# Kernel tuning notes

Measured on AMD Instinct MI355X. Metric: run time of the kernel, lower is better.

Reference implementation:

```python
import jax, jax.numpy as jnp
import numpy as np
from jax import lax

# Kernel / geometry constants matching init_kwargs
KZ, KX, KY = 9, 15, 15          # PSF support
STRIDE = (1, 1, 1)              # scale = (zscale, xscale, yscale)
Z_PAD = (KZ - 1 + 1) // 2       # 4
X_PAD = (KX - 1 + 1) // 2       # 7
Y_PAD = (KY - 1 + 1) // 2       # 7


def _dist(n):
    # |idx - n//2|, matching _distance_from_center
    return jnp.abs(jnp.arange(n, dtype=jnp.float32) - n // 2)


def gen_psf(bet_xy, bet_z, alpha):
    b = bet_xy.shape[0]
    zd = _dist(KZ)                                  # [KZ]
    xd = _dist(KX)
    yd = _dist(KY)
    # gen_distance_plane: dp[i, j] = xd[j]^2 + yd[i]^2  (shape [KY, KX])
    dp = yd[:, None] ** 2 + xd[None, :] ** 2
    # gen_2dnorm: [b, KY, KX]
    bxy = bet_xy[:, None, None]
    lat = jnp.exp(-dp[None] / (2.0 * bxy ** 2)) / (2.0 * jnp.pi * bxy ** 2)
    # gen_1dnorm: [b, KZ]
    bz = bet_z[:, None]
    ax = jnp.exp(-(zd[None] ** 2) / (2.0 * bz ** 2)) / (jnp.sqrt(2.0 * jnp.pi) * bz)
    # psf = exp(log(lateral) + log(axial)) == lateral * axial  -> [b, 1, KZ, KY, KX]
    psf = lat[:, None, None, :, :] * ax[:, None, :, None, None]
    # double_exp mode
    psf = 1.0 - jnp.exp(-alpha[:, None, None, None, None] * psf)
    return psf / jnp.sum(psf)


def reference(x, bet_xy, bet_z, alpha):
    # x: [B, 1, Z, X, Y]; original computes dense conv3d giving [B, B, ...] and
    # keeps only the diagonal _x[b, b]. That is mathematically a per-sample
    # (grouped) convolution, implemented here without the O(B) redundancy.
    psf = gen_psf(bet_xy, bet_z, alpha)             # [B, 1, KZ, KY, KX]
    B = x.shape[0]
    xin = jnp.transpose(x, (1, 0, 2, 3, 4))         # [1, B, Z, X, Y]
    out = lax.conv_general_dilated(
        xin, psf,
        window_strides=STRIDE,
        padding=[(Z_PAD, Z_PAD), (X_PAD, X_PAD), (Y_PAD, Y_PAD)],
        dimension_numbers=("NCDHW", "OIDHW", "NCDHW"),
        feature_group_count=B,
    )                                               # [1, B, Z', X', Y']
    return jnp.transpose(out, (1, 0, 2, 3, 4))      # [B, 1, Z', X', Y']


def setup_inputs() -> dict:
    key = jax.random.key(0)
    k1, k2, k3, k4 = jax.random.split(key, 4)
    B = 4
    x = jax.random.normal(k1, (B, 1, 32, 192, 192), dtype=jnp.float32)
    bet_xy = 1.0 + 2.0 * jax.random.uniform(k2, (B,), dtype=jnp.float32)   # in [1, 3)
    bet_z = 1.0 + 2.0 * jax.random.uniform(k3, (B,), dtype=jnp.float32)    # in [1, 3)
    alpha = 1.0 + 9.0 * jax.random.uniform(k4, (B,), dtype=jnp.float32)    # in [1, 10)
    return {"x": x, "bet_xy": bet_xy, "bet_z": bet_z, "alpha": alpha}
```

## Files before the change

### kernel.cpp

```cpp
#include <hip/hip_runtime.h>
#include <math.h>

#define B_ 4
#define D_ 32
#define H_ 192
#define W_ 192
#define HW_ (H_ * W_)

#define NT 5

#define TW 48
#define TH 12
#define NTHR 256
#define ZCHUNK 16
#define NP (ZCHUNK + 8)

#define XT_H 26
#define XT_COLS 62
#define XT_W 64
#define XT_CELLS (XT_H * XT_COLS)
#define NSEC 7
#define XT_SZ (XT_H * XT_W)

#define R2_PL (TH * XT_W)
#define RBUF (NT * R2_PL)

#define SMEM_WORDS (2 * XT_SZ + 2 * RBUF + 16)

#define NTAPS (B_ * 9 * 15 * 15)

__device__ inline float4 f4fma(float c, float4 a, float4 d) {
    d.x = fmaf(c, a.x, d.x); d.y = fmaf(c, a.y, d.y);
    d.z = fmaf(c, a.z, d.z); d.w = fmaf(c, a.w, d.w);
    return d;
}
__device__ inline float4 f4add(float4 a, float4 b) {
    a.x += b.x; a.y += b.y; a.z += b.z; a.w += b.w; return a;
}
__device__ inline float rfl(float x) {
    return __int_as_float(__builtin_amdgcn_readfirstlane(__float_as_int(x)));
}

__global__ __launch_bounds__(NTHR)
void conv_kernel(const float* __restrict__ x,
                 const float* __restrict__ bet_xy,
                 const float* __restrict__ bet_z,
                 const float* __restrict__ alpha,
                 float* __restrict__ out) {
    __shared__ __align__(16) float smem[SMEM_WORDS];
    float* xtb = smem;
    float* Rb  = smem + 2 * XT_SZ;
    float* red = smem;
    float* ct  = smem + 512;

    const int t  = threadIdx.x;
    const int w0 = blockIdx.x * TW;
    const int h0 = blockIdx.y * TH;
    const int bz = blockIdx.z;
    const int b  = bz & 3;
    const int z0 = (bz >> 2) * ZCHUNK;
    const float INV = 0.3989422804014327f;

    float local = 0.f;
#pragma unroll
    for (int s = 0; s < 32; ++s) {
        int idx = t + s * NTHR;
        if (idx < NTAPS) {
            int bb = idx / 2025;
            int r  = idx % 2025;
            int dz = r / 225;
            int r2 = r % 225;
            int dh = r2 / 15;
            int dw = r2 % 15;
            float bxy = bet_xy[bb], bzv = bet_z[bb], al = alpha[bb];
            float zd = (float)(dz - 4), hd = (float)(dh - 7), wd = (float)(dw - 7);
            float az = expf(-zd * zd / (2.f * bzv * bzv)) * (INV / bzv);
            float gh = expf(-hd * hd / (2.f * bxy * bxy)) * (INV / bxy);
            float gw = expf(-wd * wd / (2.f * bxy * bxy)) * (INV / bxy);
            local += 1.f - expf(-al * az * gh * gw);
        }
    }
    red[t] = local;
    __syncthreads();
    for (int s = 128; s > 0; s >>= 1) {
        if (t < s) red[t] += red[t + s];
        __syncthreads();
    }
    const float S = red[0];
    __syncthreads();

    if (t < NT * 13) {
        int n = t / 13;
        int k = t % 13;
        float bxy = bet_xy[b], bzv = bet_z[b], al = alpha[b];
        if (k < 8) {
            float d = (float)k;
            float g = expf(-d * d / (2.f * bxy * bxy)) * (INV / bxy);
            float p = g;
            for (int q = 0; q < n; ++q) p *= g;
            ct[n * 16 + k] = p;
        } else {
            float d = (float)(k - 8);
            float az = expf(-d * d / (2.f * bzv * bzv)) * (INV / bzv);
            float base = al * az;
            float p = base;
            for (int q = 0; q < n; ++q) p *= base;
            const float facs[NT] = {1.f, 2.f, 6.f, 24.f, 120.f};
            float sign = (n & 1) ? -1.f : 1.f;
            ct[n * 16 + k] = sign * p / (facs[n] * S);
        }
    }
    __syncthreads();

    float cg_[NT][8], cz_[NT][5];
#pragma unroll
    for (int n = 0; n < NT; ++n) {
#pragma unroll
        for (int k = 0; k < 8; ++k) cg_[n][k] = rfl(ct[n * 16 + k]);
#pragma unroll
        for (int k = 0; k < 5; ++k) cz_[n][k] = rfl(ct[n * 16 + 8 + k]);
    }
    __syncthreads();

    const float* xb = x + (size_t)b * (D_ * HW_);
    int goff[NSEC], loff[NSEC];
#pragma unroll
    for (int k = 0; k < NSEC; ++k) {
        int i = t + k * NTHR;
        int r = i / XT_COLS, c = i - r * XT_COLS;
        int gh = h0 + r - 7, gw = w0 + c - 7;
        bool ok = (i < XT_CELLS) && gh >= 0 && gh < H_ && gw >= 0 && gw < W_;
        goff[k] = ok ? (gh * W_ + gw) : -1;
        loff[k] = (i < XT_CELLS) ? (r * XT_W + c) : (XT_SZ - 1);
    }
    if (t < XT_H * 2) {
        int r = t >> 1, c = 62 + (t & 1);
        xtb[r * XT_W + c] = 0.f;
        xtb[XT_SZ + r * XT_W + c] = 0.f;
    }
    {
        int zi0 = z0 - 4;
        if (zi0 >= 0) {
#pragma unroll
            for (int k = 0; k < NSEC; ++k) {
                float v = 0.f;
                if (goff[k] >= 0) v = xb[(size_t)zi0 * HW_ + goff[k]];
                xtb[loff[k]] = v;
            }
        }
    }

    const int bid = blockIdx.x + (int)gridDim.x * (blockIdx.y + (int)gridDim.y * blockIdx.z);
    const int rt  = (t + ((bid & 1) << 7)) & (NTHR - 1);

    const bool s1act = (rt < 192);
    const bool s2on = (rt >= 64);
    const int l2 = rt - 64;
    const int s2ro = l2 >> 4, s2cg = l2 & 15;
    const bool s2store = s2on && (s2cg < 12);

    float4 acc[9];
#pragma unroll
    for (int k = 0; k < 9; ++k) acc[k] = make_float4(0.f, 0.f, 0.f, 0.f);

#pragma unroll 1
    for (int p = 0; p <= NP; ++p) {
        __syncthreads();

        const int zi = z0 - 4 + p;
        const bool do_s1 = (p < NP) && (zi >= 0) && (zi < D_) && s1act;
        const int  zn    = zi + 1;
        const bool pvalid = (p + 1 < NP) && (zn >= 0) && (zn < D_);

        float pv[NSEC];
        if (pvalid) {
            const float* xp = xb + (size_t)zn * HW_;
#pragma unroll
            for (int k = 0; k < NSEC; ++k) pv[k] = (goff[k] >= 0) ? xp[goff[k]] : 0.f;
        }

        if (do_s1) {
            const float4* x4 = (const float4*)(xtb + (p & 1) * XT_SZ + 4 * rt);
            float4* R4 = (float4*)(Rb + (p & 1) * RBUF) + rt;
            float4 ctr = x4[7 * 16];
            float4 sp[7];
#pragma unroll
            for (int k = 1; k <= 7; ++k)
                sp[k - 1] = f4add(x4[(7 - k) * 16], x4[(7 + k) * 16]);
#pragma unroll
            for (int n = 0; n < NT; ++n) {
                float c0 = cg_[n][0];
                float4 a;
                a.x = c0 * ctr.x; a.y = c0 * ctr.y;
                a.z = c0 * ctr.z; a.w = c0 * ctr.w;
#pragma unroll
                for (int k = 1; k <= 7; ++k) a = f4fma(cg_[n][k], sp[k - 1], a);
                R4[n * (R2_PL / 4)] = a;
            }
        }

        if (p >= 1 && s2on) {
            const int ziq = zi - 1;
            if (ziq >= 0 && ziq < D_) {
                const float4* R4 = (const float4*)(Rb + ((p - 1) & 1) * RBUF) + l2;
#pragma unroll
                for (int n = 0; n < NT; ++n) {
                    float win[20];
#pragma unroll
                    for (int i = 0; i < 5; ++i) {
                        float4 a = R4[n * (R2_PL / 4) + i];
                        win[4 * i]     = a.x; win[4 * i + 1] = a.y;
                        win[4 * i + 2] = a.z; win[4 * i + 3] = a.w;
                    }
                    float c0 = cg_[n][0];
                    float4 qv;
                    qv.x = c0 * win[7];  qv.y = c0 * win[8];
                    qv.z = c0 * win[9];  qv.w = c0 * win[10];
#pragma unroll
                    for (int k = 1; k <= 7; ++k) {
                        float c = cg_[n][k];
                        qv.x = fmaf(c, win[7 - k]  + win[7 + k],  qv.x);
                        qv.y = fmaf(c, win[8 - k]  + win[8 + k],  qv.y);
                        qv.z = fmaf(c, win[9 - k]  + win[9 + k],  qv.z);
                        qv.w = fmaf(c, win[10 - k] + win[10 + k], qv.w);
                    }
                    acc[4] = f4fma(cz_[n][0], qv, acc[4]);
#pragma unroll
                    for (int j = 1; j <= 4; ++j) {
                        float cz = cz_[n][j];
                        acc[4 + j] = f4fma(cz, qv, acc[4 + j]);
                        acc[4 - j] = f4fma(cz, qv, acc[4 - j]);
                    }
                }
            }
            if (p - 1 >= 8 && s2store) {
                int z = z0 + (p - 1 - 8);
                size_t o = ((size_t)(b * D_ + z) * H_ + (h0 + s2ro)) * W_ + (w0 + 4 * s2cg);
                *(float4*)&out[o] = acc[0];
            }
#pragma unroll
            for (int k = 0; k < 8; ++k) acc[k] = acc[k + 1];
            acc[8] = make_float4(0.f, 0.f, 0.f, 0.f);
        }

        if (pvalid) {
            float* xn = xtb + ((p + 1) & 1) * XT_SZ;
#pragma unroll
            for (int k = 0; k < NSEC; ++k) xn[loff[k]] = pv[k];
        }
    }
}

extern "C" void kernel_launch(void* const* d_in, const int* in_sizes, int n_in,
                              void* d_out, int out_size, void* d_ws, size_t ws_size,
                              hipStream_t stream) {
    const float* x      = (const float*)d_in[0];
    const float* bet_xy = (const float*)d_in[1];
    const float* bet_z  = (const float*)d_in[2];
    const float* alpha  = (const float*)d_in[3];
    float* out = (float*)d_out;

    hipLaunchKernelGGL(conv_kernel, dim3(W_ / TW, H_ / TH, B_ * (D_ / ZCHUNK)),
                       dim3(NTHR), 0, stream, x, bet_xy, bet_z, alpha, out);
}
```

Measured before the change: 159.8 us.

## Load input rows directly from global into registers, drop shared input tile, halve z-chunk

Stage 1 of the separable convolution now reads its 15 vertical taps straight from global memory as float4 loads into registers, so the double-buffered shared-memory input tile and its scalar staging stores are gone. Block size drops to 192 threads and every thread runs both stages, with the z-accumulation folded into a local 5-term sum before it is added to the rolling accumulators. The z-chunk is halved, which doubles the number of blocks but raises the share of z-halo work. The cost is redundant global/L2 reads of overlapping rows and columns, and loads that are no longer prefetched a plane ahead.

```diff
diff --git a/kernel.cpp b/kernel.cpp
--- a/kernel.cpp
+++ b/kernel.cpp
@@ -11,21 +11,15 @@
 
 #define TW 48
 #define TH 12
-#define NTHR 256
-#define ZCHUNK 16
+#define NTHR 192
+#define ZCHUNK 8
 #define NP (ZCHUNK + 8)
 
-#define XT_H 26
-#define XT_COLS 62
-#define XT_W 64
-#define XT_CELLS (XT_H * XT_COLS)
-#define NSEC 7
-#define XT_SZ (XT_H * XT_W)
-
-#define R2_PL (TH * XT_W)
-#define RBUF (NT * R2_PL)
-
-#define SMEM_WORDS (2 * XT_SZ + 2 * RBUF + 16)
+#define RQ 16
+#define RW 64
+#define R_PL (TH * RW)
+#define RBUF (NT * R_PL)
+#define SMEM_WORDS (2 * RBUF + 16)
 
 #define NTAPS (B_ * 9 * 15 * 15)
 
@@ -48,8 +42,7 @@
                  const float* __restrict__ alpha,
                  float* __restrict__ out) {
     __shared__ __align__(16) float smem[SMEM_WORDS];
-    float* xtb = smem;
-    float* Rb  = smem + 2 * XT_SZ;
+    float* Rb  = smem;
     float* red = smem;
     float* ct  = smem + 512;
 
@@ -60,10 +53,11 @@
     const int b  = bz & 3;
     const int z0 = (bz >> 2) * ZCHUNK;
     const float INV = 0.3989422804014327f;
+    const float4 z4 = make_float4(0.f, 0.f, 0.f, 0.f);
 
     float local = 0.f;
 #pragma unroll
-    for (int s = 0; s < 32; ++s) {
+    for (int s = 0; s < 43; ++s) {
         int idx = t + s * NTHR;
         if (idx < NTAPS) {
             int bb = idx / 2025;
@@ -83,7 +77,7 @@
     red[t] = local;
     __syncthreads();
     for (int s = 128; s > 0; s >>= 1) {
-        if (t < s) red[t] += red[t + s];
+        if (t < s && t + s < NTHR) red[t] += red[t + s];
         __syncthreads();
     }
     const float S = red[0];
@@ -122,71 +116,108 @@
     }
     __syncthreads();
 
+    const int r1 = t >> 4;
+    const int q  = t & 15;
+    const int gc0 = w0 - 8 + 4 * q;
+    const bool qok = (gc0 >= 0) && (gc0 <= W_ - 4);
+    const int gcc = min(max(gc0, 0), W_ - 4);
+    const int rbase = h0 + r1 - 7;
+    const bool hint = (h0 >= 7) && (h0 + TH + 6 <= H_ - 1);
     const float* xb = x + (size_t)b * (D_ * HW_);
-    int goff[NSEC], loff[NSEC];
-#pragma unroll
-    for (int k = 0; k < NSEC; ++k) {
-        int i = t + k * NTHR;
-        int r = i / XT_COLS, c = i - r * XT_COLS;
-        int gh = h0 + r - 7, gw = w0 + c - 7;
-        bool ok = (i < XT_CELLS) && gh >= 0 && gh < H_ && gw >= 0 && gw < W_;
-        goff[k] = ok ? (gh * W_ + gw) : -1;
-        loff[k] = (i < XT_CELLS) ? (r * XT_W + c) : (XT_SZ - 1);
-    }
-    if (t < XT_H * 2) {
-        int r = t >> 1, c = 62 + (t & 1);
-        xtb[r * XT_W + c] = 0.f;
-        xtb[XT_SZ + r * XT_W + c] = 0.f;
-    }
-    {
-        int zi0 = z0 - 4;
-        if (zi0 >= 0) {
-#pragma unroll
-            for (int k = 0; k < NSEC; ++k) {
-                float v = 0.f;
-                if (goff[k] >= 0) v = xb[(size_t)zi0 * HW_ + goff[k]];
-                xtb[loff[k]] = v;
-            }
-        }
-    }
-
-    const int bid = blockIdx.x + (int)gridDim.x * (blockIdx.y + (int)gridDim.y * blockIdx.z);
-    const int rt  = (t + ((bid & 1) << 7)) & (NTHR - 1);
-
-    const bool s1act = (rt < 192);
-    const bool s2on = (rt >= 64);
-    const int l2 = rt - 64;
-    const int s2ro = l2 >> 4, s2cg = l2 & 15;
-    const bool s2store = s2on && (s2cg < 12);
 
     float4 acc[9];
 #pragma unroll
-    for (int k = 0; k < 9; ++k) acc[k] = make_float4(0.f, 0.f, 0.f, 0.f);
+    for (int k = 0; k < 9; ++k) acc[k] = z4;
 
 #pragma unroll 1
     for (int p = 0; p <= NP; ++p) {
         __syncthreads();
 
         const int zi = z0 - 4 + p;
-        const bool do_s1 = (p < NP) && (zi >= 0) && (zi < D_) && s1act;
-        const int  zn    = zi + 1;
-        const bool pvalid = (p + 1 < NP) && (zn >= 0) && (zn < D_);
-
-        float pv[NSEC];
-        if (pvalid) {
-            const float* xp = xb + (size_t)zn * HW_;
-#pragma unroll
-            for (int k = 0; k < NSEC; ++k) pv[k] = (goff[k] >= 0) ? xp[goff[k]] : 0.f;
-        }
-
+        const bool do_s1 = (p < NP) && (zi >= 0) && (zi < D_);
+
+        float4 pv[15];
         if (do_s1) {
-            const float4* x4 = (const float4*)(xtb + (p & 1) * XT_SZ + 4 * rt);
-            float4* R4 = (float4*)(Rb + (p & 1) * RBUF) + rt;
-            float4 ctr = x4[7 * 16];
+            const float* pl = xb + (size_t)zi * HW_ + gcc;
+            if (hint) {
+                const float* pr = pl + (size_t)rbase * W_;
+#pragma unroll
+                for (int dh = 0; dh < 15; ++dh)
+                    pv[dh] = *(const float4*)(pr + (size_t)dh * W_);
+            } else {
+#pragma unroll
+                for (int dh = 0; dh < 15; ++dh) {
+                    int gr = rbase + dh;
+                    int grc = min(max(gr, 0), H_ - 1);
+                    float4 v = *(const float4*)(pl + (size_t)grc * W_);
+                    pv[dh] = ((unsigned)gr < (unsigned)H_) ? v : z4;
+                }
+            }
+        }
+
+        if (p >= 1) {
+            const int ziq = zi - 1;
+            if (ziq >= 0 && ziq < D_) {
+                const float4* R4 = (const float4*)(Rb + ((p - 1) & 1) * RBUF);
+                float4 u[5];
+#pragma unroll
+                for (int n = 0; n < NT; ++n) {
+                    float win[20];
+#pragma unroll
+                    for (int i = 0; i < 5; ++i) {
+                        float4 a = R4[n * (R_PL / 4) + t + i];
+                        win[4 * i]     = a.x; win[4 * i + 1] = a.y;
+                        win[4 * i + 2] = a.z; win[4 * i + 3] = a.w;
+                    }
+                    float c0 = cg_[n][0];
+                    float4 qv;
+                    qv.x = c0 * win[8];  qv.y = c0 * win[9];
+                    qv.z = c0 * win[10]; qv.w = c0 * win[11];
+#pragma unroll
+                    for (int k = 1; k <= 7; ++k) {
+                        float c = cg_[n][k];
+                        qv.x = fmaf(c, win[8 - k]  + win[8 + k],  qv.x);
+                        qv.y = fmaf(c, win[9 - k]  + win[9 + k],  qv.y);
+                        qv.z = fmaf(c, win[10 - k] + win[10 + k], qv.z);
+                        qv.w = fmaf(c, win[11 - k] + win[11 + k], qv.w);
+                    }
+                    if (n == 0) {
+#pragma unroll
+                        for (int j = 0; j < 5; ++j) {
+                            float cz = cz_[0][j];
+                            u[j].x = cz * qv.x; u[j].y = cz * qv.y;
+                            u[j].z = cz * qv.z; u[j].w = cz * qv.w;
+                        }
+                    } else {
+#pragma unroll
+                        for (int j = 0; j < 5; ++j)
+                            u[j] = f4fma(cz_[n][j], qv, u[j]);
+                    }
+                }
+                acc[4] = f4add(acc[4], u[0]);
+#pragma unroll
+                for (int j = 1; j <= 4; ++j) {
+                    acc[4 + j] = f4add(acc[4 + j], u[j]);
+                    acc[4 - j] = f4add(acc[4 - j], u[j]);
+                }
+            }
+            if (p - 1 >= 8 && q < 12) {
+                int z = z0 + (p - 1 - 8);
+                size_t o = ((size_t)(b * D_ + z) * H_ + (h0 + r1)) * W_ + (w0 + 4 * q);
+                *(float4*)&out[o] = acc[0];
+            }
+#pragma unroll
+            for (int k = 0; k < 8; ++k) acc[k] = acc[k + 1];
+            acc[8] = z4;
+        }
+
+        if (do_s1) {
+            float4 ctr = pv[7];
             float4 sp[7];
 #pragma unroll
             for (int k = 1; k <= 7; ++k)
-                sp[k - 1] = f4add(x4[(7 - k) * 16], x4[(7 + k) * 16]);
+                sp[k - 1] = f4add(pv[7 - k], pv[7 + k]);
+            float4* R4w = (float4*)(Rb + (p & 1) * RBUF);
 #pragma unroll
             for (int n = 0; n < NT; ++n) {
                 float c0 = cg_[n][0];
@@ -195,58 +226,8 @@
                 a.z = c0 * ctr.z; a.w = c0 * ctr.w;
 #pragma unroll
                 for (int k = 1; k <= 7; ++k) a = f4fma(cg_[n][k], sp[k - 1], a);
-                R4[n * (R2_PL / 4)] = a;
-            }
-        }
-
-        if (p >= 1 && s2on) {
-            const int ziq = zi - 1;
-            if (ziq >= 0 && ziq < D_) {
-                const float4* R4 = (const float4*)(Rb + ((p - 1) & 1) * RBUF) + l2;
-#pragma unroll
-                for (int n = 0; n < NT; ++n) {
-                    float win[20];
-#pragma unroll
-                    for (int i = 0; i < 5; ++i) {
-                        float4 a = R4[n * (R2_PL / 4) + i];
-                        win[4 * i]     = a.x; win[4 * i + 1] = a.y;
-                        win[4 * i + 2] = a.z; win[4 * i + 3] = a.w;
-                    }
-                    float c0 = cg_[n][0];
-                    float4 qv;
-                    qv.x = c0 * win[7];  qv.y = c0 * win[8];
-                    qv.z = c0 * win[9];  qv.w = c0 * win[10];
-#pragma unroll
-                    for (int k = 1; k <= 7; ++k) {
-                        float c = cg_[n][k];
-                        qv.x = fmaf(c, win[7 - k]  + win[7 + k],  qv.x);
-                        qv.y = fmaf(c, win[8 - k]  + win[8 + k],  qv.y);
-                        qv.z = fmaf(c, win[9 - k]  + win[9 + k],  qv.z);
-                        qv.w = fmaf(c, win[10 - k] + win[10 + k], qv.w);
-                    }
-                    acc[4] = f4fma(cz_[n][0], qv, acc[4]);
-#pragma unroll
-                    for (int j = 1; j <= 4; ++j) {
-                        float cz = cz_[n][j];
-                        acc[4 + j] = f4fma(cz, qv, acc[4 + j]);
-                        acc[4 - j] = f4fma(cz, qv, acc[4 - j]);
-                    }
-                }
-            }
-            if (p - 1 >= 8 && s2store) {
-                int z = z0 + (p - 1 - 8);
-                size_t o = ((size_t)(b * D_ + z) * H_ + (h0 + s2ro)) * W_ + (w0 + 4 * s2cg);
-                *(float4*)&out[o] = acc[0];
-            }
-#pragma unroll
-            for (int k = 0; k < 8; ++k) acc[k] = acc[k + 1];
-            acc[8] = make_float4(0.f, 0.f, 0.f, 0.f);
-        }
-
-        if (pvalid) {
-            float* xn = xtb + ((p + 1) & 1) * XT_SZ;
-#pragma unroll
-            for (int k = 0; k < NSEC; ++k) xn[loff[k]] = pv[k];
+                R4w[n * (R_PL / 4) + t] = qok ? a : z4;
+            }
         }
     }
 }
```

Result: slower. 342.5 us (+114.4%).
